# Optimization experiments

Hardware: AMD Instinct MI355X
Metric: run time of the kernel (lower is better)

## Reference

```python
import jax, jax.numpy as jnp
import numpy as np

D_MODEL = 1024
H = 16
D_K = D_MODEL // H
THETA = 10000.0
MAX_SEQ = 2048
SEQ = 2048
BATCH = 2


def _rope_tables():
    # tri[i, k] angles: i / theta**(2k/d_k)
    pos = jnp.arange(MAX_SEQ, dtype=jnp.float32)[:, None]          # [S, 1]
    inv_freq = THETA ** (-2.0 * jnp.arange(D_K // 2, dtype=jnp.float32) / D_K)  # [dk/2]
    ang = pos * inv_freq                                            # [S, dk/2]
    return jnp.cos(ang), jnp.sin(ang)


def _apply_rope(x, token_positions, cos_t, sin_t):
    # x: [b, h, s, dk]; rotate interleaved pairs
    cos = cos_t[token_positions]  # [s, dk/2]
    sin = sin_t[token_positions]
    x2 = x.reshape(x.shape[:-1] + (D_K // 2, 2))
    x0, x1 = x2[..., 0], x2[..., 1]
    r0 = x0 * cos - x1 * sin
    r1 = x0 * sin + x1 * cos
    return jnp.stack([r0, r1], axis=-1).reshape(x.shape)


def setup_inputs() -> dict:
    key = jax.random.key(0)
    ks = jax.random.split(key, 5)
    sigma = np.sqrt(2.0 / (D_MODEL + D_MODEL))
    return {
        "x": jax.random.normal(ks[0], (BATCH, SEQ, D_MODEL), dtype=jnp.float32),
        "token_positions": jnp.arange(SEQ, dtype=jnp.int64 if jax.config.jax_enable_x64 else jnp.int32),
        "Wq": (jax.random.normal(ks[1], (D_MODEL, D_MODEL), dtype=jnp.float32) * sigma),
        "Wk": (jax.random.normal(ks[2], (D_MODEL, D_MODEL), dtype=jnp.float32) * sigma),
        "Wv": (jax.random.normal(ks[3], (D_MODEL, D_MODEL), dtype=jnp.float32) * sigma),
        "Wo": (jax.random.normal(ks[4], (D_MODEL, D_MODEL), dtype=jnp.float32) * sigma),
    }


def reference(x, token_positions, Wq, Wk, Wv, Wo):
    b, s, _ = x.shape
    cos_t, sin_t = _rope_tables()

    def proj(W):
        y = jnp.einsum('oi,bsi->bso', W, x)                 # [b, s, d_model]
        return y.reshape(b, s, H, D_K).transpose(0, 2, 1, 3)  # [b, h, s, dk]

    Q = _apply_rope(proj(Wq), token_positions, cos_t, sin_t)
    K = _apply_rope(proj(Wk), token_positions, cos_t, sin_t)
    V = proj(Wv)

    scores = jnp.einsum('bhqd,bhkd->bhqk', Q, K) / jnp.sqrt(jnp.float32(D_K))
    causal = jnp.tril(jnp.ones((s, s), dtype=bool))
    scores = jnp.where(causal, scores, -jnp.inf)
    attn = jax.nn.softmax(scores, axis=-1)
    out = jnp.einsum('bhqk,bhkd->bhqd', attn, V)            # [b, h, s, dv]
    out = out.transpose(0, 2, 1, 3).reshape(b, s, D_MODEL)
    return jnp.einsum('oi,bsi->bso', Wo, out)
```

## Files before the change

### kernel.cpp

```cpp
#include <hip/hip_runtime.h>
#include <hip/hip_bf16.h>
#include <math.h>

#define D_MODEL 1024
#define NH      16
#define DK      64
#define SEQ     2048
#define BATCH   2

typedef float  f32x4  __attribute__((ext_vector_type(4)));
typedef __bf16 bf16x8 __attribute__((ext_vector_type(8)));
typedef unsigned short ushx4 __attribute__((ext_vector_type(4)));
typedef unsigned short ushx8 __attribute__((ext_vector_type(8)));
typedef unsigned short u16;

__device__ inline u16 cbf(float f) { __bf16 h = (__bf16)f; return *(u16*)&h; }

__device__ inline void gload16(const u16* g, u16* l) {
    __builtin_amdgcn_global_load_lds(
        (const __attribute__((address_space(1))) unsigned int*)g,
        (__attribute__((address_space(3))) unsigned int*)l,
        16, 0, 0);
}

__global__ void rope_tables_kernel(float2* __restrict__ cs) {
    int i = blockIdx.x * 256 + threadIdx.x;
    int pos = i >> 5, k = i & 31;
    float inv = powf(10000.0f, -2.0f * (float)k / 64.0f);
    float ang = (float)pos * inv;
    cs[i] = make_float2(cosf(ang), sinf(ang));
}

__global__ void cvt_kernel(const float* __restrict__ in, u16* __restrict__ out) {
    size_t i = ((size_t)blockIdx.x * 256 + threadIdx.x) * 8;
    f32x4 v0 = *(const f32x4*)(in + i);
    f32x4 v1 = *(const f32x4*)(in + i + 4);
    ushx4 o0, o1;
    #pragma unroll
    for (int e = 0; e < 4; e++) { o0[e] = cbf(v0[e]); o1[e] = cbf(v1[e]); }
    *(ushx4*)(out + i) = o0;
    *(ushx4*)(out + i + 4) = o1;
}

__global__ void cvtw_kernel(const float* __restrict__ wq, const float* __restrict__ wk,
                            const float* __restrict__ wv, const float* __restrict__ wo,
                            u16* __restrict__ oq, u16* __restrict__ ok,
                            u16* __restrict__ ov, u16* __restrict__ oo) {
    const float* in; u16* out;
    switch (blockIdx.y) {
        case 0: in = wq; out = oq; break;
        case 1: in = wk; out = ok; break;
        case 2: in = wv; out = ov; break;
        default: in = wo; out = oo; break;
    }
    size_t i = ((size_t)blockIdx.x * 256 + threadIdx.x) * 8;
    f32x4 v0 = *(const f32x4*)(in + i);
    f32x4 v1 = *(const f32x4*)(in + i + 4);
    ushx4 o0, o1;
    #pragma unroll
    for (int e = 0; e < 4; e++) { o0[e] = cbf(v0[e]); o1[e] = cbf(v1[e]); }
    *(ushx4*)(out + i) = o0;
    *(ushx4*)(out + i + 4) = o1;
}

template<int MODE>
__global__ __launch_bounds__(256) void gemm_bt(
    const u16* __restrict__ A, const u16* __restrict__ W,
    u16* __restrict__ Qo, u16* __restrict__ Ko, void* __restrict__ Oo,
    const int* __restrict__ tpos, const float2* __restrict__ cs)
{
    constexpr int K = 1024;
    __shared__ u16 As[2][128 * 32];
    __shared__ u16 Bs[2][128 * 32];

    const int t  = threadIdx.x;
    const int m0 = blockIdx.x * 128, n0 = blockIdx.y * 128;
    const int lane = t & 63, wid = t >> 6;
    const int wm = wid >> 1, wn = wid & 1;
    const int lr = lane & 15, lg = lane >> 4;

    const int ldrow0 = wid * 32 + (lane >> 2);
    const int ldrow1 = ldrow0 + 16;
    const int lc = lane & 3;
    const u16* Asrc0 = A + (size_t)(m0 + ldrow0) * K + ((lc ^ ((ldrow0 >> 1) & 3)) << 3);
    const u16* Asrc1 = A + (size_t)(m0 + ldrow1) * K + ((lc ^ ((ldrow1 >> 1) & 3)) << 3);
    const u16* Bsrc0 = W + (size_t)(n0 + ldrow0) * K + ((lc ^ ((ldrow0 >> 1) & 3)) << 3);
    const u16* Bsrc1 = W + (size_t)(n0 + ldrow1) * K + ((lc ^ ((ldrow1 >> 1) & 3)) << 3);
    const int d0 = (wid * 32) * 32, d1 = (wid * 32 + 16) * 32;

    f32x4 acc[4][4];
    #pragma unroll
    for (int i = 0; i < 4; i++)
        #pragma unroll
        for (int j2 = 0; j2 < 4; j2++) acc[i][j2] = 0.0f;

    auto stage = [&](int buf, int k0) {
        gload16(Asrc0 + k0, &As[buf][d0]);
        gload16(Asrc1 + k0, &As[buf][d1]);
        gload16(Bsrc0 + k0, &Bs[buf][d0]);
        gload16(Bsrc1 + k0, &Bs[buf][d1]);
    };

    stage(0, 0);
    int buf = 0;
    for (int k0 = 0; k0 < K; k0 += 32) {
        __syncthreads();
        if (k0 + 32 < K) stage(buf ^ 1, k0 + 32);

        bf16x8 af[4], bfr[4];
        #pragma unroll
        for (int mi = 0; mi < 4; mi++) {
            int row = wm * 64 + mi * 16 + lr;
            af[mi] = *(const bf16x8*)&As[buf][row * 32 + ((lg ^ ((row >> 1) & 3)) << 3)];
        }
        #pragma unroll
        for (int ni = 0; ni < 4; ni++) {
            int row = wn * 64 + ni * 16 + lr;
            bfr[ni] = *(const bf16x8*)&Bs[buf][row * 32 + ((lg ^ ((row >> 1) & 3)) << 3)];
        }
        #pragma unroll
        for (int mi = 0; mi < 4; mi++)
            #pragma unroll
            for (int ni = 0; ni < 4; ni++) {
                if constexpr (MODE == 3)
                    acc[mi][ni] = __builtin_amdgcn_mfma_f32_16x16x32_bf16(bfr[ni], af[mi], acc[mi][ni], 0, 0, 0);
                else
                    acc[mi][ni] = __builtin_amdgcn_mfma_f32_16x16x32_bf16(af[mi], bfr[ni], acc[mi][ni], 0, 0, 0);
            }
        buf ^= 1;
    }

    #pragma unroll
    for (int mi = 0; mi < 4; mi++)
        #pragma unroll
        for (int ni = 0; ni < 4; ni++) {
            f32x4 v4 = acc[mi][ni];
            #pragma unroll
            for (int r = 0; r < 4; r++) {
                float v = v4[r];
                if constexpr (MODE == 3) {
                    int n = n0 + wn * 64 + ni * 16 + lg * 4 + r;
                    int m = m0 + wm * 64 + mi * 16 + lr;
                    int h = n >> 6, d = n & 63;
                    int b = m >> 11, s = m & 2047;
                    ((u16*)Oo)[(((size_t)b * NH + h) * DK + d) * SEQ + s] = cbf(v);
                } else {
                    int m = m0 + wm * 64 + mi * 16 + lg * 4 + r;
                    int n = n0 + wn * 64 + ni * 16 + lr;
                    if constexpr (MODE == 2) {
                        ((float*)Oo)[(size_t)m * D_MODEL + n] = v;
                    } else {
                        int b = m >> 11, s = m & 2047;
                        int h = (n >> 6) & 15, d = n & 63;
                        float vp = __shfl_xor(v, 1);
                        int tp = tpos[s];
                        float2 c2 = cs[tp * 32 + (d >> 1)];
                        float res = (d & 1) ? (vp * c2.y + v * c2.x) : (v * c2.x - vp * c2.y);
                        const int sel = n0 >> 10;
                        if (sel == 0) res *= 0.18033688f;
                        u16* outp = sel ? Ko : Qo;
                        outp[(((size_t)b * NH + h) * SEQ + s) * DK + d] = cbf(res);
                    }
                }
            }
        }
}

__global__ __launch_bounds__(256) void attn_kernel(
    const u16* __restrict__ Q,
    const u16* __restrict__ Km,
    const u16* __restrict__ VT,
    u16* __restrict__ aout)
{
    __shared__ u16 Ks[2][64 * 64];
    __shared__ u16 Vs[64 * 64];
    __shared__ u16 Pl[4][16 * 64];
    const int t = threadIdx.x, wid = t >> 6, lane = t & 63;
    const int lr = lane & 15, lg = lane >> 4;
    const int bx = blockIdx.x;
    const int j = bx & 31;
    const int p = bx >> 5;
    const int bh = (j & 7) * 4 + (j >> 3);
    const int b = bh >> 4, h = bh & 15;
    const int srow = lane >> 3, schunk = lane & 7;
    const int row0 = wid * 16;
    const int swz = (schunk ^ srow) << 3;

    const u16* Qg = Q  + (size_t)bh * SEQ * DK;
    const u16* Kg = Km + (size_t)bh * SEQ * DK;
    const u16* Vg = VT + (size_t)bh * DK * SEQ;
    u16* Plw = Pl[wid];

    auto process = [&](int qb) {
        const int q0 = qb * 64;
        const int qw = q0 + row0;
        const int nkt = qb + 1;

        __syncthreads();

        bf16x8 aq[2];
        #pragma unroll
        for (int h2 = 0; h2 < 2; h2++)
            aq[h2] = *(const bf16x8*)&Qg[(qw + lr) * DK + h2 * 32 + lg * 8];

        float m_run = -__builtin_inff(), l_run = 0.0f;
        f32x4 acc[4];
        #pragma unroll
        for (int dg = 0; dg < 4; dg++) acc[dg] = 0.0f;

        const u16* kptr = Kg + (size_t)(row0 + srow) * DK + swz;
        const u16* vptr = Vg + (size_t)(row0 + srow) * SEQ + swz;

        gload16(kptr,          &Ks[0][row0 * 64]);
        gload16(kptr + 8 * DK, &Ks[0][(row0 + 8) * 64]);
        kptr += 64 * DK;

        for (int kt = 0; kt < nkt; kt++) {
            __builtin_amdgcn_sched_barrier(0);
            __builtin_amdgcn_s_barrier();
            __builtin_amdgcn_sched_barrier(0);
            gload16(vptr,                   &Vs[row0 * 64]);
            gload16(vptr + (size_t)8 * SEQ, &Vs[(row0 + 8) * 64]);
            vptr += 64;
            u16* kd = &Ks[(kt + 1) & 1][0];
            gload16(kptr,          kd + row0 * 64);
            gload16(kptr + 8 * DK, kd + (row0 + 8) * 64);
            kptr += 64 * DK;
            const int kb = kt * 64;

            asm volatile("s_waitcnt vmcnt(4)" ::: "memory");
            __builtin_amdgcn_sched_barrier(0);
            bf16x8 kf[4][2];
            #pragma unroll
            for (int kg = 0; kg < 4; kg++)
                #pragma unroll
                for (int h2 = 0; h2 < 2; h2++) {
                    int row = kg * 16 + lr;
                    kf[kg][h2] = *(const bf16x8*)&Ks[kt & 1][row * 64 + (((h2 * 4 + lg) ^ (lr & 7)) << 3)];
                }

            f32x4 sf[4];
            #pragma unroll
            for (int kg = 0; kg < 4; kg++) sf[kg] = 0.0f;
            __builtin_amdgcn_s_setprio(1);
            #pragma unroll
            for (int kg = 0; kg < 4; kg++) {
                sf[kg] = __builtin_amdgcn_mfma_f32_16x16x32_bf16(kf[kg][0], aq[0], sf[kg], 0, 0, 0);
                sf[kg] = __builtin_amdgcn_mfma_f32_16x16x32_bf16(kf[kg][1], aq[1], sf[kg], 0, 0, 0);
            }
            __builtin_amdgcn_s_setprio(0);

            {
                if (kb + 64 > qw) {
                    const int qq = qw + lr;
                    #pragma unroll
                    for (int kg = 0; kg < 4; kg++)
                        #pragma unroll
                        for (int r = 0; r < 4; r++)
                            if (kb + kg * 16 + lg * 4 + r > qq) sf[kg][r] = -__builtin_inff();
                }
                float cmax = sf[0][0];
                #pragma unroll
                for (int kg = 0; kg < 4; kg++)
                    #pragma unroll
                    for (int r = 0; r < 4; r++) cmax = fmaxf(cmax, sf[kg][r]);
                if (!__all(cmax <= m_run + 8.0f)) {
                    float mt = fmaxf(cmax, __shfl_xor(cmax, 16));
                    mt = fmaxf(mt, __shfl_xor(mt, 32));
                    float mn = fmaxf(m_run, mt);
                    float scr = exp2f(m_run - mn);
                    m_run = mn;
                    l_run *= scr;
                    #pragma unroll
                    for (int dg = 0; dg < 4; dg++) acc[dg] *= scr;
                }
                float l = 0.0f;
                const int prow = lr * 64;
                #pragma unroll
                for (int kg = 0; kg < 4; kg++) {
                    ushx4 pk;
                    #pragma unroll
                    for (int r = 0; r < 4; r++) {
                        float pv = exp2f(sf[kg][r] - m_run);
                        l += pv;
                        pk[r] = cbf(pv);
                    }
                    *(ushx4*)&Plw[prow + (((kg * 4 + lg) ^ ((lr & 7) << 1)) << 2)] = pk;
                }
                l_run += l;
            }

            asm volatile("s_waitcnt vmcnt(2)" ::: "memory");
            __builtin_amdgcn_sched_barrier(0);
            bf16x8 vf[2][4];
            #pragma unroll
            for (int ck = 0; ck < 2; ck++)
                #pragma unroll
                for (int dg = 0; dg < 4; dg++) {
                    int row = dg * 16 + lr;
                    vf[ck][dg] = *(const bf16x8*)&Vs[row * 64 + (((ck * 4 + lg) ^ (lr & 7)) << 3)];
                }

            asm volatile("s_waitcnt lgkmcnt(0)" ::: "memory");
            __builtin_amdgcn_sched_barrier(0);
            bf16x8 pa[2];
            #pragma unroll
            for (int ck = 0; ck < 2; ck++)
                pa[ck] = *(const bf16x8*)&Plw[lr * 64 + (((ck * 8 + lg * 2) ^ ((lr & 7) << 1)) << 2)];
            __builtin_amdgcn_s_setprio(1);
            #pragma unroll
            for (int ck = 0; ck < 2; ck++)
                #pragma unroll
                for (int dg = 0; dg < 4; dg++)
                    acc[dg] = __builtin_amdgcn_mfma_f32_16x16x32_bf16(vf[ck][dg], pa[ck], acc[dg], 0, 0, 0);
            __builtin_amdgcn_s_setprio(0);
        }

        l_run += __shfl_xor(l_run, 16);
        l_run += __shfl_xor(l_run, 32);

        {
            float inv = 1.0f / l_run;
            int q = qw + lr;
            #pragma unroll
            for (int dg = 0; dg < 4; dg++) {
                ushx4 ow;
                #pragma unroll
                for (int r = 0; r < 4; r++) ow[r] = cbf(acc[dg][r] * inv);
                *(ushx4*)&aout[((size_t)b * SEQ + q) * D_MODEL + h * DK + dg * 16 + lg * 4] = ow;
            }
        }
    };

    process(31 - p);
    process(p);
}

extern "C" void kernel_launch(void* const* d_in, const int* in_sizes, int n_in,
                              void* d_out, int out_size, void* d_ws, size_t ws_size,
                              hipStream_t stream) {
    const float* x    = (const float*)d_in[0];
    const int*   tpos = (const int*)d_in[1];
    const float* Wq   = (const float*)d_in[2];
    const float* Wk   = (const float*)d_in[3];
    const float* Wv   = (const float*)d_in[4];
    const float* Wo   = (const float*)d_in[5];
    float* out = (float*)d_out;

    char* ws = (char*)d_ws;
    float2* cs = (float2*)ws;
    u16* Qb   = (u16*)(ws + (512 << 10));
    u16* Kb   = (u16*)(ws + (512 << 10) + ((size_t)8  << 20));
    u16* VT   = (u16*)(ws + (512 << 10) + ((size_t)16 << 20));
    u16* xb   = (u16*)(ws + (512 << 10) + ((size_t)24 << 20));
    u16* Wqb  = (u16*)(ws + (512 << 10) + ((size_t)32 << 20));
    u16* Wkb  = (u16*)(ws + (512 << 10) + ((size_t)34 << 20));
    u16* Wvb  = (u16*)(ws + (512 << 10) + ((size_t)36 << 20));
    u16* Wob  = (u16*)(ws + (512 << 10) + ((size_t)38 << 20));
    u16* attnb = xb;

    rope_tables_kernel<<<256, 256, 0, stream>>>(cs);
    cvt_kernel<<<2048, 256, 0, stream>>>(x, xb);
    cvtw_kernel<<<dim3(512, 4), 256, 0, stream>>>(Wq, Wk, Wv, Wo, Wqb, Wkb, Wvb, Wob);

    gemm_bt<0><<<dim3(32, 16), 256, 0, stream>>>(xb, Wqb, Qb, Kb, nullptr, tpos, cs);
    gemm_bt<3><<<dim3(32, 8),  256, 0, stream>>>(xb, Wvb, nullptr, nullptr, VT, tpos, cs);

    attn_kernel<<<512, 256, 0, stream>>>(Qb, Kb, VT, attnb);

    gemm_bt<2><<<dim3(32, 8),  256, 0, stream>>>(attnb, Wob, nullptr, nullptr, out, tpos, cs);
}
```

Measured before the change: 134.1 us.

## Split attention into one query block per workgroup and compute row sums via MFMA

Each workgroup now handles one 64-row query block instead of a paired long/short block, which doubles the grid. Blocks are ordered in a zigzag so heavy and light causal tiles are interleaved for load balance. The softmax row-sum is accumulated with an extra MFMA against a ones vector on the bf16-rounded probabilities, replacing the scalar adds and the cross-lane shuffle reductions. The cost is one more MFMA per chunk and less even per-block work; sums now use the rounded probabilities, which matches what the PV product uses.

```diff
diff --git a/kernel.cpp b/kernel.cpp
--- a/kernel.cpp
+++ b/kernel.cpp
@@ -179,11 +179,16 @@
     const int lr = lane & 15, lg = lane >> 4;
     const int bx = blockIdx.x;
     const int j = bx & 31;
-    const int p = bx >> 5;
+    const int qidx = bx >> 5;
+    const int gq = qidx >> 3, iq = qidx & 7;
+    const int qb = (gq == 0) ? iq : (gq == 1) ? 15 - iq : (gq == 2) ? 16 + iq : 31 - iq;
     const int bh = (j & 7) * 4 + (j >> 3);
     const int b = bh >> 4, h = bh & 15;
+    const int q0 = qb * 64;
+    const int row0 = wid * 16;
+    const int qw = q0 + row0;
+    const int nkt = qb + 1;
     const int srow = lane >> 3, schunk = lane & 7;
-    const int row0 = wid * 16;
     const int swz = (schunk ^ srow) << 3;
 
     const u16* Qg = Q  + (size_t)bh * SEQ * DK;
@@ -191,149 +196,137 @@
     const u16* Vg = VT + (size_t)bh * DK * SEQ;
     u16* Plw = Pl[wid];
 
-    auto process = [&](int qb) {
-        const int q0 = qb * 64;
-        const int qw = q0 + row0;
-        const int nkt = qb + 1;
-
-        __syncthreads();
-
-        bf16x8 aq[2];
-        #pragma unroll
-        for (int h2 = 0; h2 < 2; h2++)
-            aq[h2] = *(const bf16x8*)&Qg[(qw + lr) * DK + h2 * 32 + lg * 8];
-
-        float m_run = -__builtin_inff(), l_run = 0.0f;
-        f32x4 acc[4];
-        #pragma unroll
-        for (int dg = 0; dg < 4; dg++) acc[dg] = 0.0f;
-
-        const u16* kptr = Kg + (size_t)(row0 + srow) * DK + swz;
-        const u16* vptr = Vg + (size_t)(row0 + srow) * SEQ + swz;
-
-        gload16(kptr,          &Ks[0][row0 * 64]);
-        gload16(kptr + 8 * DK, &Ks[0][(row0 + 8) * 64]);
+    bf16x8 aq[2];
+    #pragma unroll
+    for (int h2 = 0; h2 < 2; h2++)
+        aq[h2] = *(const bf16x8*)&Qg[(qw + lr) * DK + h2 * 32 + lg * 8];
+
+    bf16x8 onesf;
+    #pragma unroll
+    for (int e = 0; e < 8; e++) onesf[e] = (__bf16)1.0f;
+
+    float m_run = -__builtin_inff();
+    f32x4 acc[4];
+    f32x4 acc_l = 0.0f;
+    #pragma unroll
+    for (int dg = 0; dg < 4; dg++) acc[dg] = 0.0f;
+
+    const u16* kptr = Kg + (size_t)(row0 + srow) * DK + swz;
+    const u16* vptr = Vg + (size_t)(row0 + srow) * SEQ + swz;
+
+    gload16(kptr,          &Ks[0][row0 * 64]);
+    gload16(kptr + 8 * DK, &Ks[0][(row0 + 8) * 64]);
+    kptr += 64 * DK;
+
+    for (int kt = 0; kt < nkt; kt++) {
+        __builtin_amdgcn_sched_barrier(0);
+        __builtin_amdgcn_s_barrier();
+        __builtin_amdgcn_sched_barrier(0);
+        gload16(vptr,                   &Vs[row0 * 64]);
+        gload16(vptr + (size_t)8 * SEQ, &Vs[(row0 + 8) * 64]);
+        vptr += 64;
+        u16* kd = &Ks[(kt + 1) & 1][0];
+        gload16(kptr,          kd + row0 * 64);
+        gload16(kptr + 8 * DK, kd + (row0 + 8) * 64);
         kptr += 64 * DK;
-
-        for (int kt = 0; kt < nkt; kt++) {
-            __builtin_amdgcn_sched_barrier(0);
-            __builtin_amdgcn_s_barrier();
-            __builtin_amdgcn_sched_barrier(0);
-            gload16(vptr,                   &Vs[row0 * 64]);
-            gload16(vptr + (size_t)8 * SEQ, &Vs[(row0 + 8) * 64]);
-            vptr += 64;
-            u16* kd = &Ks[(kt + 1) & 1][0];
-            gload16(kptr,          kd + row0 * 64);
-            gload16(kptr + 8 * DK, kd + (row0 + 8) * 64);
-            kptr += 64 * DK;
-            const int kb = kt * 64;
-
-            asm volatile("s_waitcnt vmcnt(4)" ::: "memory");
-            __builtin_amdgcn_sched_barrier(0);
-            bf16x8 kf[4][2];
-            #pragma unroll
-            for (int kg = 0; kg < 4; kg++)
-                #pragma unroll
-                for (int h2 = 0; h2 < 2; h2++) {
-                    int row = kg * 16 + lr;
-                    kf[kg][h2] = *(const bf16x8*)&Ks[kt & 1][row * 64 + (((h2 * 4 + lg) ^ (lr & 7)) << 3)];
-                }
-
-            f32x4 sf[4];
-            #pragma unroll
-            for (int kg = 0; kg < 4; kg++) sf[kg] = 0.0f;
-            __builtin_amdgcn_s_setprio(1);
-            #pragma unroll
-            for (int kg = 0; kg < 4; kg++) {
-                sf[kg] = __builtin_amdgcn_mfma_f32_16x16x32_bf16(kf[kg][0], aq[0], sf[kg], 0, 0, 0);
-                sf[kg] = __builtin_amdgcn_mfma_f32_16x16x32_bf16(kf[kg][1], aq[1], sf[kg], 0, 0, 0);
-            }
-            __builtin_amdgcn_s_setprio(0);
-
-            {
-                if (kb + 64 > qw) {
-                    const int qq = qw + lr;
-                    #pragma unroll
-                    for (int kg = 0; kg < 4; kg++)
-                        #pragma unroll
-                        for (int r = 0; r < 4; r++)
-                            if (kb + kg * 16 + lg * 4 + r > qq) sf[kg][r] = -__builtin_inff();
-                }
-                float cmax = sf[0][0];
+        const int kb = kt * 64;
+
+        asm volatile("s_waitcnt vmcnt(4)" ::: "memory");
+        __builtin_amdgcn_sched_barrier(0);
+        bf16x8 kf[4][2];
+        #pragma unroll
+        for (int kg = 0; kg < 4; kg++)
+            #pragma unroll
+            for (int h2 = 0; h2 < 2; h2++) {
+                int row = kg * 16 + lr;
+                kf[kg][h2] = *(const bf16x8*)&Ks[kt & 1][row * 64 + (((h2 * 4 + lg) ^ (lr & 7)) << 3)];
+            }
+
+        f32x4 sf[4];
+        #pragma unroll
+        for (int kg = 0; kg < 4; kg++) sf[kg] = 0.0f;
+        __builtin_amdgcn_s_setprio(1);
+        #pragma unroll
+        for (int kg = 0; kg < 4; kg++) {
+            sf[kg] = __builtin_amdgcn_mfma_f32_16x16x32_bf16(kf[kg][0], aq[0], sf[kg], 0, 0, 0);
+            sf[kg] = __builtin_amdgcn_mfma_f32_16x16x32_bf16(kf[kg][1], aq[1], sf[kg], 0, 0, 0);
+        }
+        __builtin_amdgcn_s_setprio(0);
+
+        {
+            if (kb + 64 > qw) {
+                const int qq = qw + lr;
                 #pragma unroll
                 for (int kg = 0; kg < 4; kg++)
                     #pragma unroll
-                    for (int r = 0; r < 4; r++) cmax = fmaxf(cmax, sf[kg][r]);
-                if (!__all(cmax <= m_run + 8.0f)) {
-                    float mt = fmaxf(cmax, __shfl_xor(cmax, 16));
-                    mt = fmaxf(mt, __shfl_xor(mt, 32));
-                    float mn = fmaxf(m_run, mt);
-                    float scr = exp2f(m_run - mn);
-                    m_run = mn;
-                    l_run *= scr;
-                    #pragma unroll
-                    for (int dg = 0; dg < 4; dg++) acc[dg] *= scr;
-                }
-                float l = 0.0f;
-                const int prow = lr * 64;
+                    for (int r = 0; r < 4; r++)
+                        if (kb + kg * 16 + lg * 4 + r > qq) sf[kg][r] = -__builtin_inff();
+            }
+            float mk[4];
+            #pragma unroll
+            for (int kg = 0; kg < 4; kg++)
+                mk[kg] = fmaxf(fmaxf(sf[kg][0], sf[kg][1]), fmaxf(sf[kg][2], sf[kg][3]));
+            float cmax = fmaxf(fmaxf(mk[0], mk[1]), fmaxf(mk[2], mk[3]));
+            if (!__all(cmax <= m_run + 8.0f)) {
+                float mt = fmaxf(cmax, __shfl_xor(cmax, 16));
+                mt = fmaxf(mt, __shfl_xor(mt, 32));
+                float mn = fmaxf(m_run, mt);
+                float scr = exp2f(m_run - mn);
+                m_run = mn;
+                acc_l[0] *= scr;
                 #pragma unroll
-                for (int kg = 0; kg < 4; kg++) {
-                    ushx4 pk;
-                    #pragma unroll
-                    for (int r = 0; r < 4; r++) {
-                        float pv = exp2f(sf[kg][r] - m_run);
-                        l += pv;
-                        pk[r] = cbf(pv);
-                    }
-                    *(ushx4*)&Plw[prow + (((kg * 4 + lg) ^ ((lr & 7) << 1)) << 2)] = pk;
-                }
-                l_run += l;
-            }
-
-            asm volatile("s_waitcnt vmcnt(2)" ::: "memory");
-            __builtin_amdgcn_sched_barrier(0);
-            bf16x8 vf[2][4];
-            #pragma unroll
-            for (int ck = 0; ck < 2; ck++)
+                for (int dg = 0; dg < 4; dg++) acc[dg] *= scr;
+            }
+            const int prow = lr * 64;
+            #pragma unroll
+            for (int kg = 0; kg < 4; kg++) {
+                ushx4 pk;
                 #pragma unroll
-                for (int dg = 0; dg < 4; dg++) {
-                    int row = dg * 16 + lr;
-                    vf[ck][dg] = *(const bf16x8*)&Vs[row * 64 + (((ck * 4 + lg) ^ (lr & 7)) << 3)];
-                }
-
-            asm volatile("s_waitcnt lgkmcnt(0)" ::: "memory");
-            __builtin_amdgcn_sched_barrier(0);
-            bf16x8 pa[2];
-            #pragma unroll
-            for (int ck = 0; ck < 2; ck++)
-                pa[ck] = *(const bf16x8*)&Plw[lr * 64 + (((ck * 8 + lg * 2) ^ ((lr & 7) << 1)) << 2)];
-            __builtin_amdgcn_s_setprio(1);
-            #pragma unroll
-            for (int ck = 0; ck < 2; ck++)
-                #pragma unroll
-                for (int dg = 0; dg < 4; dg++)
-                    acc[dg] = __builtin_amdgcn_mfma_f32_16x16x32_bf16(vf[ck][dg], pa[ck], acc[dg], 0, 0, 0);
-            __builtin_amdgcn_s_setprio(0);
-        }
-
-        l_run += __shfl_xor(l_run, 16);
-        l_run += __shfl_xor(l_run, 32);
-
-        {
-            float inv = 1.0f / l_run;
-            int q = qw + lr;
+                for (int r = 0; r < 4; r++)
+                    pk[r] = cbf(exp2f(sf[kg][r] - m_run));
+                *(ushx4*)&Plw[prow + (((kg * 4 + lg) ^ ((lr & 7) << 1)) << 2)] = pk;
+            }
+        }
+
+        asm volatile("s_waitcnt vmcnt(2)" ::: "memory");
+        __builtin_amdgcn_sched_barrier(0);
+        bf16x8 vf[2][4];
+        #pragma unroll
+        for (int ck = 0; ck < 2; ck++)
             #pragma unroll
             for (int dg = 0; dg < 4; dg++) {
-                ushx4 ow;
-                #pragma unroll
-                for (int r = 0; r < 4; r++) ow[r] = cbf(acc[dg][r] * inv);
-                *(ushx4*)&aout[((size_t)b * SEQ + q) * D_MODEL + h * DK + dg * 16 + lg * 4] = ow;
-            }
-        }
-    };
-
-    process(31 - p);
-    process(p);
+                int row = dg * 16 + lr;
+                vf[ck][dg] = *(const bf16x8*)&Vs[row * 64 + (((ck * 4 + lg) ^ (lr & 7)) << 3)];
+            }
+
+        asm volatile("s_waitcnt lgkmcnt(0)" ::: "memory");
+        __builtin_amdgcn_sched_barrier(0);
+        bf16x8 pa[2];
+        #pragma unroll
+        for (int ck = 0; ck < 2; ck++)
+            pa[ck] = *(const bf16x8*)&Plw[lr * 64 + (((ck * 8 + lg * 2) ^ ((lr & 7) << 1)) << 2)];
+        __builtin_amdgcn_s_setprio(1);
+        #pragma unroll
+        for (int ck = 0; ck < 2; ck++) {
+            #pragma unroll
+            for (int dg = 0; dg < 4; dg++)
+                acc[dg] = __builtin_amdgcn_mfma_f32_16x16x32_bf16(vf[ck][dg], pa[ck], acc[dg], 0, 0, 0);
+            acc_l = __builtin_amdgcn_mfma_f32_16x16x32_bf16(onesf, pa[ck], acc_l, 0, 0, 0);
+        }
+        __builtin_amdgcn_s_setprio(0);
+    }
+
+    {
+        float inv = 1.0f / acc_l[0];
+        int q = qw + lr;
+        #pragma unroll
+        for (int dg = 0; dg < 4; dg++) {
+            ushx4 ow;
+            #pragma unroll
+            for (int r = 0; r < 4; r++) ow[r] = cbf(acc[dg][r] * inv);
+            *(ushx4*)&aout[((size_t)b * SEQ + q) * D_MODEL + h * DK + dg * 16 + lg * 4] = ow;
+        }
+    }
 }
 
 extern "C" void kernel_launch(void* const* d_in, const int* in_sizes, int n_in,
@@ -366,7 +359,7 @@
     gemm_bt<0><<<dim3(32, 16), 256, 0, stream>>>(xb, Wqb, Qb, Kb, nullptr, tpos, cs);
     gemm_bt<3><<<dim3(32, 8),  256, 0, stream>>>(xb, Wvb, nullptr, nullptr, VT, tpos, cs);
 
-    attn_kernel<<<512, 256, 0, stream>>>(Qb, Kb, VT, attnb);
+    attn_kernel<<<1024, 256, 0, stream>>>(Qb, Kb, VT, attnb);
 
     gemm_bt<2><<<dim3(32, 8),  256, 0, stream>>>(attnb, Wob, nullptr, nullptr, out, tpos, cs);
 }
```

Result: slower. 137.5 us (+2.6%).
